# Kernel tuning notes

Hardware: AMD Instinct MI355X
Metric: run time of the kernel (lower is better)

Reference implementation:

```python
import jax, jax.numpy as jnp
import numpy as np

B, N, P, C, H = 8, 512, 16, 512, 8
HD = C // H  # 64


def setup_inputs() -> dict:
    key = jax.random.key(0)
    k1, k2, k3, k4, k5 = jax.random.split(key, 5)
    x = jax.random.normal(k1, (B, N, P, C), dtype=jnp.float32)
    # binary observation mask; force slot 0 valid so masked mean never divides by 0
    mask = (jax.random.uniform(k2, (B, N, P)) > 0.3).astype(jnp.float32)
    mask = mask.at[:, :, 0].set(1.0)
    lens = jax.random.randint(k3, (B,), 1, N)
    lens_mask = jnp.ones((B, N), dtype=jnp.float32)
    # parameters (torch Linear stored as [in, out] here; qkv_bias=False, proj has bias)
    Wqkv = jax.random.normal(k4, (C, 3 * C), dtype=jnp.float32) * (1.0 / np.sqrt(C))
    Wproj = jax.random.normal(k5, (C, C), dtype=jnp.float32) * (1.0 / np.sqrt(C))
    bproj = jnp.zeros((C,), dtype=jnp.float32)
    return {"x": x, "mask": mask, "lens": lens, "lens_mask": lens_mask,
            "Wqkv": Wqkv, "Wproj": Wproj, "bproj": bproj}


def reference(x, mask, lens, lens_mask, Wqkv, Wproj, bproj):
    # lens / lens_mask are unused by the original forward
    b, n, p, c = x.shape
    h, hd = H, c // H
    qkv = jnp.einsum('bnpc,cd->bnpd', x, Wqkv).reshape(b, n, p, 3, h, hd)
    # q: take P-slot 0                       -> [B,H,N,hd]
    q = qkv[:, :, 0, 0].transpose(0, 2, 1, 3)
    # k: masked mean over P                  -> [B,H,N,hd]
    m = mask[..., None, None]                      # [B,N,P,1,1]
    k = (jnp.where(m > 0, qkv[:, :, :, 1], 0.0).sum(axis=2) / m.sum(axis=2))
    k = k.transpose(0, 2, 1, 3)
    # v: pack P into channel dim             -> [B,H,N,hd*P]
    v = qkv[:, :, :, 2].transpose(0, 3, 1, 4, 2).reshape(b, h, n, hd * p)
    # SDPA over N (scale by 1/sqrt(head_dim of q))
    scale = 1.0 / np.sqrt(hd)
    attn = jax.nn.softmax(jnp.einsum('bhnd,bhmd->bhnm', q, k) * scale, axis=-1)
    out = jnp.einsum('bhnm,bhme->bhne', attn, v)            # [B,H,N,hd*P]
    # unpack P back out                       -> [B,N,P,C]
    out = out.reshape(b, h, n, hd, p).transpose(0, 2, 4, 1, 3).reshape(b, n, p, c)
    return out @ Wproj + bproj
```

## Files before the change

kernel.cpp:

```cpp
#include <hip/hip_runtime.h>

typedef _Float16 f16;
typedef __attribute__((ext_vector_type(8))) _Float16 half8;
typedef __attribute__((ext_vector_type(2))) _Float16 half2v;
typedef __attribute__((ext_vector_type(4))) float float4v;

#define MODE_QK 0
#define MODE_V 1
#define MODE_PV 2
#define MODE_PROJ 3


__device__ __forceinline__ void gload16(const f16* g, f16* l) {
    __builtin_amdgcn_global_load_lds(
        (const __attribute__((address_space(1))) void*)g,
        (__attribute__((address_space(3))) void*)l, 16, 0, 0);
}

__global__ __launch_bounds__(256) void wt_kernel(const float* __restrict__ Wqkv,
    const float* __restrict__ Wproj, f16* __restrict__ WT, f16* __restrict__ WpT)
{
    int idx = blockIdx.x * 256 + threadIdx.x;
    if (idx < 1536 * 512) {
        int d = idx >> 9, c = idx & 511;
        WT[idx] = (f16)Wqkv[c * 1536 + d];
    } else {
        int i2 = idx - 1536 * 512;
        int d = i2 >> 9, c = i2 & 511;
        WpT[i2] = (f16)Wproj[c * 512 + d];
    }
}

__global__ __launch_bounds__(256) void xprep_kernel(const float* __restrict__ x,
    const float* __restrict__ mask, f16* __restrict__ xf, f16* __restrict__ xmean)
{
    int bn = blockIdx.x;
    int t = threadIdx.x;
    const float* xrow = x + (size_t)bn * 16 * 512;
    const float* mrow = mask + (size_t)bn * 16;
    float msum = 0.f;
    #pragma unroll
    for (int p = 0; p < 16; p++) msum += mrow[p];
    int c = t * 2;
    float a0 = 0.f, a1 = 0.f;
    #pragma unroll
    for (int p = 0; p < 16; p++) {
        float2 v = *(const float2*)(xrow + p * 512 + c);
        float m = mrow[p];
        a0 += m * v.x; a1 += m * v.y;
        half2v h; h[0] = (f16)v.x; h[1] = (f16)v.y;
        *(half2v*)(xf + (size_t)bn * 16 * 512 + p * 512 + c) = h;
    }
    float inv = 1.f / msum;
    half2v hm; hm[0] = (f16)(a0 * inv); hm[1] = (f16)(a1 * inv);
    *(half2v*)(xmean + (size_t)bn * 512 + c) = hm;
}

template<int MODE>
__global__ __launch_bounds__(256) void gemm128(
    const f16* __restrict__ pA, const f16* __restrict__ pA2,
    const f16* __restrict__ pB,
    f16* __restrict__ outa, f16* __restrict__ outb,
    float* __restrict__ outf, const float* __restrict__ bias)
{
    __shared__ f16 As[128 * 32];
    __shared__ f16 Bs[128 * 32];
    const int t = threadIdx.x;
    const int lane = t & 63;
    const int w = t >> 6;
    const int wm = w & 1, wn = w >> 1;
    const int quad = lane >> 4, l15 = lane & 15;

    const int n0 = blockIdx.x * 128;
    const int m0 = blockIdx.y * 128;
    int vb = 0, vp = 0, z = 0;

    const f16* Abase; size_t sA;
    const f16* Bbase; size_t sB;
    if constexpr (MODE == MODE_QK) {
        if (n0 < 512) { Abase = pA;  sA = 8192; }
        else          { Abase = pA2; sA = 512;  }
        Bbase = pB; sB = 512;
    } else if constexpr (MODE == MODE_V) {
        z = blockIdx.z; vb = z >> 4; vp = z & 15;
        Abase = pA; sA = 512;
        Bbase = pB + ((size_t)vb * 512 * 16 + vp) * 512; sB = 8192;
    } else if constexpr (MODE == MODE_PV) {
        z = blockIdx.z;
        Abase = pA + (size_t)z * 512 * 512; sA = 512;
        Bbase = pB + (size_t)z * 1024 * 512; sB = 512;
    } else {
        Abase = pA; sA = 512;
        Bbase = pB; sB = 512;
    }

    const int rlo = (lane >> 2), kof = (lane & 3) * 8;
    const f16* ga0 = Abase + (size_t)(m0 + w * 16 + rlo) * sA + kof;
    const f16* ga1 = Abase + (size_t)(m0 + (w + 4) * 16 + rlo) * sA + kof;
    const f16* gb0 = Bbase + (size_t)(n0 + w * 16 + rlo) * sB + kof;
    const f16* gb1 = Bbase + (size_t)(n0 + (w + 4) * 16 + rlo) * sB + kof;
    f16* lA0 = As + w * 512;
    f16* lA1 = As + (w + 4) * 512;
    f16* lB0 = Bs + w * 512;
    f16* lB1 = Bs + (w + 4) * 512;

    float4v acc[4][4];
    #pragma unroll
    for (int i = 0; i < 4; i++)
        #pragma unroll
        for (int j = 0; j < 4; j++)
            acc[i][j] = (float4v){0.f, 0.f, 0.f, 0.f};

    for (int kt = 0; kt < 16; kt++) {
        __syncthreads();
        gload16(ga0, lA0); gload16(ga1, lA1);
        gload16(gb0, lB0); gload16(gb1, lB1);
        ga0 += 32; ga1 += 32; gb0 += 32; gb1 += 32;
        __syncthreads();
        half8 af[4], bf[4];
        #pragma unroll
        for (int mi = 0; mi < 4; mi++)
            af[mi] = *(const half8*)&As[(wm * 64 + mi * 16 + l15) * 32 + quad * 8];
        #pragma unroll
        for (int ni = 0; ni < 4; ni++)
            bf[ni] = *(const half8*)&Bs[(wn * 64 + ni * 16 + l15) * 32 + quad * 8];
        #pragma unroll
        for (int mi = 0; mi < 4; mi++)
            #pragma unroll
            for (int ni = 0; ni < 4; ni++)
                acc[mi][ni] = __builtin_amdgcn_mfma_f32_16x16x32_f16(
                    af[mi], bf[ni], acc[mi][ni], 0, 0, 0);
    }

    #pragma unroll
    for (int mi = 0; mi < 4; mi++) {
        #pragma unroll
        for (int ni = 0; ni < 4; ni++) {
            #pragma unroll
            for (int i = 0; i < 4; i++) {
                int lrow = wm * 64 + mi * 16 + quad * 4 + i;
                int lcol = wn * 64 + ni * 16 + l15;
                float val = acc[mi][ni][i];
                if constexpr (MODE == MODE_QK) {
                    int gm = m0 + lrow, gj = n0 + lcol;
                    int b = gm >> 9, n = gm & 511;
                    if (gj < 512)
                        outa[(((size_t)(b * 8 + (gj >> 6))) * 512 + n) * 64 + (gj & 63)] = (f16)val;
                    else {
                        int jj = gj - 512;
                        outb[(((size_t)(b * 8 + (jj >> 6))) * 512 + n) * 64 + (jj & 63)] = (f16)val;
                    }
                } else if constexpr (MODE == MODE_V) {
                    int gi = m0 + lrow, gn = n0 + lcol;
                    int h = gi >> 6, dd = gi & 63;
                    outa[(((size_t)(vb * 8 + h)) * 1024 + vp * 64 + dd) * 512 + gn] = (f16)val;
                } else if constexpr (MODE == MODE_PV) {
                    int n = m0 + lrow, e = n0 + lcol;
                    int p = e >> 6, dd = e & 63;
                    int b = z >> 3, h = z & 7;
                    outa[((size_t)(b * 512 + n) * 16 + p) * 512 + h * 64 + dd] = (f16)val;
                } else {
                    outf[(size_t)(m0 + lrow) * 512 + (n0 + lcol)] = val + bias[n0 + lcol];
                }
            }
        }
    }
}

__global__ __launch_bounds__(256) void qk_softmax_kernel(
    const f16* __restrict__ q, const f16* __restrict__ k, f16* __restrict__ Pout)
{
    __shared__ f16 qs[64 * 72];
    __shared__ f16 ks[512 * 72];
    const int t = threadIdx.x;
    const int bh = blockIdx.y;
    const int n0 = blockIdx.x * 64;
    #pragma unroll
    for (int i = 0; i < 2; i++) {
        int cid = i * 256 + t;
        int row = cid >> 3, off = (cid & 7) * 8;
        *(half8*)&qs[row * 72 + off] =
            *(const half8*)&q[((size_t)bh * 512 + n0 + row) * 64 + off];
    }
    #pragma unroll
    for (int i = 0; i < 16; i++) {
        int cid = i * 256 + t;
        int row = cid >> 3, off = (cid & 7) * 8;
        *(half8*)&ks[row * 72 + off] =
            *(const half8*)&k[((size_t)bh * 512 + row) * 64 + off];
    }
    __syncthreads();
    const int lane = t & 63, w = t >> 6;
    const int quad = lane >> 4, l15 = lane & 15;
    const int qrow = w * 16 + l15;
    half8 a0 = *(const half8*)&qs[qrow * 72 + quad * 8];
    half8 a1 = *(const half8*)&qs[qrow * 72 + 32 + quad * 8];
    float4v acc[32];
    #pragma unroll
    for (int f = 0; f < 32; f++) {
        int krow = f * 16 + l15;
        half8 b0 = *(const half8*)&ks[krow * 72 + quad * 8];
        half8 b1 = *(const half8*)&ks[krow * 72 + 32 + quad * 8];
        float4v c = {0.f, 0.f, 0.f, 0.f};
        c = __builtin_amdgcn_mfma_f32_16x16x32_f16(a0, b0, c, 0, 0, 0);
        c = __builtin_amdgcn_mfma_f32_16x16x32_f16(a1, b1, c, 0, 0, 0);
        acc[f] = c;
    }
    float mx0 = -3e38f, mx1 = -3e38f, mx2 = -3e38f, mx3 = -3e38f;
    #pragma unroll
    for (int f = 0; f < 32; f++) {
        mx0 = fmaxf(mx0, acc[f][0]); mx1 = fmaxf(mx1, acc[f][1]);
        mx2 = fmaxf(mx2, acc[f][2]); mx3 = fmaxf(mx3, acc[f][3]);
    }
    #pragma unroll
    for (int off = 1; off < 16; off <<= 1) {
        mx0 = fmaxf(mx0, __shfl_xor(mx0, off));
        mx1 = fmaxf(mx1, __shfl_xor(mx1, off));
        mx2 = fmaxf(mx2, __shfl_xor(mx2, off));
        mx3 = fmaxf(mx3, __shfl_xor(mx3, off));
    }
    float s0 = 0.f, s1 = 0.f, s2 = 0.f, s3 = 0.f;
    #pragma unroll
    for (int f = 0; f < 32; f++) {
        float e0 = __expf(0.125f * (acc[f][0] - mx0));
        float e1 = __expf(0.125f * (acc[f][1] - mx1));
        float e2 = __expf(0.125f * (acc[f][2] - mx2));
        float e3 = __expf(0.125f * (acc[f][3] - mx3));
        acc[f][0] = e0; acc[f][1] = e1; acc[f][2] = e2; acc[f][3] = e3;
        s0 += e0; s1 += e1; s2 += e2; s3 += e3;
    }
    #pragma unroll
    for (int off = 1; off < 16; off <<= 1) {
        s0 += __shfl_xor(s0, off);
        s1 += __shfl_xor(s1, off);
        s2 += __shfl_xor(s2, off);
        s3 += __shfl_xor(s3, off);
    }
    float r0 = 1.f / s0, r1 = 1.f / s1, r2 = 1.f / s2, r3 = 1.f / s3;
    size_t base = ((size_t)bh * 512 + n0 + w * 16) * 512;
    #pragma unroll
    for (int f = 0; f < 32; f++) {
        int col = f * 16 + l15;
        Pout[base + (size_t)(quad * 4 + 0) * 512 + col] = (f16)(acc[f][0] * r0);
        Pout[base + (size_t)(quad * 4 + 1) * 512 + col] = (f16)(acc[f][1] * r1);
        Pout[base + (size_t)(quad * 4 + 2) * 512 + col] = (f16)(acc[f][2] * r2);
        Pout[base + (size_t)(quad * 4 + 3) * 512 + col] = (f16)(acc[f][3] * r3);
    }
}

extern "C" void kernel_launch(void* const* d_in, const int* in_sizes, int n_in,
                              void* d_out, int out_size, void* d_ws, size_t ws_size,
                              hipStream_t stream)
{
    (void)in_sizes; (void)n_in; (void)out_size; (void)ws_size;
    const float* x     = (const float*)d_in[0];
    const float* mask  = (const float*)d_in[1];
    const float* Wqkv  = (const float*)d_in[4];
    const float* Wproj = (const float*)d_in[5];
    const float* bproj = (const float*)d_in[6];
    float* out = (float*)d_out;
    char* ws = (char*)d_ws;

    f16* xf16  = (f16*)(ws + 0);
    f16* vT    = (f16*)(ws + 67108864);
    f16* xmean = (f16*)(ws + 134217728);
    f16* WT    = (f16*)(ws + 138412032);
    f16* WpT   = (f16*)(ws + 139984896);
    f16* qb    = (f16*)(ws + 140509184);
    f16* kb    = (f16*)(ws + 144703488);
    f16* Pm    = (f16*)(ws + 148897792);
    f16* ypre  = xf16;

    wt_kernel<<<dim3(4096), dim3(256), 0, stream>>>(Wqkv, Wproj, WT, WpT);
    xprep_kernel<<<dim3(4096), dim3(256), 0, stream>>>(x, mask, xf16, xmean);
    gemm128<MODE_QK><<<dim3(8, 32), dim3(256), 0, stream>>>(
        xf16, xmean, WT, qb, kb, nullptr, nullptr);
    gemm128<MODE_V><<<dim3(4, 4, 128), dim3(256), 0, stream>>>(
        WT + 1024 * 512, nullptr, xf16, vT, nullptr, nullptr, nullptr);
    qk_softmax_kernel<<<dim3(8, 64), dim3(256), 0, stream>>>(qb, kb, Pm);
    gemm128<MODE_PV><<<dim3(8, 4, 64), dim3(256), 0, stream>>>(
        Pm, nullptr, vT, ypre, nullptr, nullptr, nullptr);
    gemm128<MODE_PROJ><<<dim3(4, 512), dim3(256), 0, stream>>>(
        ypre, nullptr, WpT, nullptr, nullptr, out, bproj);
}
```

Measured before the change: 442.7 us.

## Stage GEMM and softmax epilogues through LDS for vectorized stores; merge prep kernels

The GEMM epilogue now writes accumulators into shared memory and stores 16-byte vectors to global memory in place of scattered 2-byte stores. The projection output is written as float4 with the bias added. The QK-softmax kernel streams K in chunks through a swizzled LDS buffer using global_load_lds, and writes P through LDS staging so the stores are coalesced. The two preprocessing kernels are merged into one launch. In exchange the epilogues gain extra syncthreads and LDS round trips.

```diff
diff --git a/kernel.cpp b/kernel.cpp
--- a/kernel.cpp
+++ b/kernel.cpp
@@ -17,23 +17,24 @@
         (__attribute__((address_space(3))) void*)l, 16, 0, 0);
 }
 
-__global__ __launch_bounds__(256) void wt_kernel(const float* __restrict__ Wqkv,
-    const float* __restrict__ Wproj, f16* __restrict__ WT, f16* __restrict__ WpT)
+__global__ __launch_bounds__(256) void prep_kernel(
+    const float* __restrict__ x, const float* __restrict__ mask,
+    const float* __restrict__ Wqkv, const float* __restrict__ Wproj,
+    f16* __restrict__ xf, f16* __restrict__ xmean,
+    f16* __restrict__ WT, f16* __restrict__ WpT)
 {
-    int idx = blockIdx.x * 256 + threadIdx.x;
-    if (idx < 1536 * 512) {
-        int d = idx >> 9, c = idx & 511;
-        WT[idx] = (f16)Wqkv[c * 1536 + d];
-    } else {
-        int i2 = idx - 1536 * 512;
-        int d = i2 >> 9, c = i2 & 511;
-        WpT[i2] = (f16)Wproj[c * 512 + d];
-    }
-}
-
-__global__ __launch_bounds__(256) void xprep_kernel(const float* __restrict__ x,
-    const float* __restrict__ mask, f16* __restrict__ xf, f16* __restrict__ xmean)
-{
+    if (blockIdx.x >= 4096) {
+        int idx = (blockIdx.x - 4096) * 256 + threadIdx.x;
+        if (idx < 1536 * 512) {
+            int d = idx >> 9, c = idx & 511;
+            WT[idx] = (f16)Wqkv[c * 1536 + d];
+        } else {
+            int i2 = idx - 1536 * 512;
+            int d = i2 >> 9, c = i2 & 511;
+            WpT[i2] = (f16)Wproj[c * 512 + d];
+        }
+        return;
+    }
     int bn = blockIdx.x;
     int t = threadIdx.x;
     const float* xrow = x + (size_t)bn * 16 * 512;
@@ -63,8 +64,9 @@
     f16* __restrict__ outa, f16* __restrict__ outb,
     float* __restrict__ outf, const float* __restrict__ bias)
 {
-    __shared__ f16 As[128 * 32];
-    __shared__ f16 Bs[128 * 32];
+    __shared__ __align__(16) f16 sm[8192];
+    f16* As = sm;
+    f16* Bs = sm + 4096;
     const int t = threadIdx.x;
     const int lane = t & 63;
     const int w = t >> 6;
@@ -132,37 +134,73 @@
                     af[mi], bf[ni], acc[mi][ni], 0, 0, 0);
     }
 
-    #pragma unroll
-    for (int mi = 0; mi < 4; mi++) {
-        #pragma unroll
-        for (int ni = 0; ni < 4; ni++) {
+    __syncthreads();
+
+    if constexpr (MODE == MODE_PROJ) {
+        float* pf = (float*)sm;
+        const int rp = t >> 4, cp = (t & 15) * 8;
+        float4v bb0 = *(const float4v*)&bias[n0 + cp];
+        float4v bb1 = *(const float4v*)&bias[n0 + cp + 4];
+        #pragma unroll
+        for (int ci = 0; ci < 8; ci++) {
+            if (wm == (ci >> 2)) {
+                int mi = ci & 3;
+                #pragma unroll
+                for (int ni = 0; ni < 4; ni++)
+                    #pragma unroll
+                    for (int i = 0; i < 4; i++)
+                        pf[(quad * 4 + i) * 132 + wn * 64 + ni * 16 + l15] =
+                            acc[mi][ni][i];
+            }
+            __syncthreads();
+            float4v v0 = *(const float4v*)&pf[rp * 132 + cp];
+            float4v v1 = *(const float4v*)&pf[rp * 132 + cp + 4];
+            size_t gb = (size_t)(m0 + ci * 16 + rp) * 512 + n0 + cp;
+            *(float4v*)&outf[gb] = v0 + bb0;
+            *(float4v*)&outf[gb + 4] = v1 + bb1;
+            __syncthreads();
+        }
+    } else {
+        f16* ph = sm;
+        const int rp = t >> 3, cp = (t & 7) * 16;
+        #pragma unroll
+        for (int ci = 0; ci < 4; ci++) {
+            if (wm == (ci >> 1)) {
+                #pragma unroll
+                for (int mh = 0; mh < 2; mh++) {
+                    int mi = (ci & 1) * 2 + mh;
+                    #pragma unroll
+                    for (int ni = 0; ni < 4; ni++)
+                        #pragma unroll
+                        for (int i = 0; i < 4; i++)
+                            ph[(mh * 16 + quad * 4 + i) * 136 + wn * 64 + ni * 16 + l15] =
+                                (f16)acc[mi][ni][i];
+                }
+            }
+            __syncthreads();
+            int gr = m0 + ci * 32 + rp;
             #pragma unroll
-            for (int i = 0; i < 4; i++) {
-                int lrow = wm * 64 + mi * 16 + quad * 4 + i;
-                int lcol = wn * 64 + ni * 16 + l15;
-                float val = acc[mi][ni][i];
+            for (int s = 0; s < 2; s++) {
+                half8 v = *(const half8*)&ph[rp * 136 + cp + s * 8];
+                int gc = n0 + cp + s * 8;
                 if constexpr (MODE == MODE_QK) {
-                    int gm = m0 + lrow, gj = n0 + lcol;
-                    int b = gm >> 9, n = gm & 511;
-                    if (gj < 512)
-                        outa[(((size_t)(b * 8 + (gj >> 6))) * 512 + n) * 64 + (gj & 63)] = (f16)val;
+                    int b = gr >> 9, n = gr & 511;
+                    if (gc < 512)
+                        *(half8*)&outa[(((size_t)(b * 8 + (gc >> 6))) * 512 + n) * 64 + (gc & 63)] = v;
                     else {
-                        int jj = gj - 512;
-                        outb[(((size_t)(b * 8 + (jj >> 6))) * 512 + n) * 64 + (jj & 63)] = (f16)val;
+                        int jj = gc - 512;
+                        *(half8*)&outb[(((size_t)(b * 8 + (jj >> 6))) * 512 + n) * 64 + (jj & 63)] = v;
                     }
                 } else if constexpr (MODE == MODE_V) {
-                    int gi = m0 + lrow, gn = n0 + lcol;
-                    int h = gi >> 6, dd = gi & 63;
-                    outa[(((size_t)(vb * 8 + h)) * 1024 + vp * 64 + dd) * 512 + gn] = (f16)val;
-                } else if constexpr (MODE == MODE_PV) {
-                    int n = m0 + lrow, e = n0 + lcol;
-                    int p = e >> 6, dd = e & 63;
+                    int h = gr >> 6, dd = gr & 63;
+                    *(half8*)&outa[(((size_t)(vb * 8 + h)) * 1024 + vp * 64 + dd) * 512 + gc] = v;
+                } else {
+                    int p = gc >> 6, dd = gc & 63;
                     int b = z >> 3, h = z & 7;
-                    outa[((size_t)(b * 512 + n) * 16 + p) * 512 + h * 64 + dd] = (f16)val;
-                } else {
-                    outf[(size_t)(m0 + lrow) * 512 + (n0 + lcol)] = val + bias[n0 + lcol];
+                    *(half8*)&outa[((size_t)(b * 512 + gr) * 16 + p) * 512 + h * 64 + dd] = v;
                 }
             }
+            __syncthreads();
         }
     }
 }
@@ -170,42 +208,47 @@
 __global__ __launch_bounds__(256) void qk_softmax_kernel(
     const f16* __restrict__ q, const f16* __restrict__ k, f16* __restrict__ Pout)
 {
-    __shared__ f16 qs[64 * 72];
-    __shared__ f16 ks[512 * 72];
+    __shared__ __align__(16) f16 sm[16896];
     const int t = threadIdx.x;
+    const int lane = t & 63, w = t >> 6;
+    const int quad = lane >> 4, l15 = lane & 15;
     const int bh = blockIdx.y;
     const int n0 = blockIdx.x * 64;
-    #pragma unroll
-    for (int i = 0; i < 2; i++) {
-        int cid = i * 256 + t;
-        int row = cid >> 3, off = (cid & 7) * 8;
-        *(half8*)&qs[row * 72 + off] =
-            *(const half8*)&q[((size_t)bh * 512 + n0 + row) * 64 + off];
-    }
-    #pragma unroll
-    for (int i = 0; i < 16; i++) {
-        int cid = i * 256 + t;
-        int row = cid >> 3, off = (cid & 7) * 8;
-        *(half8*)&ks[row * 72 + off] =
-            *(const half8*)&k[((size_t)bh * 512 + row) * 64 + off];
-    }
-    __syncthreads();
-    const int lane = t & 63, w = t >> 6;
-    const int quad = lane >> 4, l15 = lane & 15;
-    const int qrow = w * 16 + l15;
-    half8 a0 = *(const half8*)&qs[qrow * 72 + quad * 8];
-    half8 a1 = *(const half8*)&qs[qrow * 72 + 32 + quad * 8];
+
+    const f16* kbase = k + (size_t)bh * 512 * 64;
+    const f16* qp = q + ((size_t)bh * 512 + n0 + w * 16 + l15) * 64 + quad * 8;
+    half8 a0 = *(const half8*)qp;
+    half8 a1 = *(const half8*)(qp + 32);
+
     float4v acc[32];
     #pragma unroll
-    for (int f = 0; f < 32; f++) {
-        int krow = f * 16 + l15;
-        half8 b0 = *(const half8*)&ks[krow * 72 + quad * 8];
-        half8 b1 = *(const half8*)&ks[krow * 72 + 32 + quad * 8];
-        float4v c = {0.f, 0.f, 0.f, 0.f};
-        c = __builtin_amdgcn_mfma_f32_16x16x32_f16(a0, b0, c, 0, 0, 0);
-        c = __builtin_amdgcn_mfma_f32_16x16x32_f16(a1, b1, c, 0, 0, 0);
-        acc[f] = c;
-    }
+    for (int f = 0; f < 32; f++) acc[f] = (float4v){0.f, 0.f, 0.f, 0.f};
+
+    const int srow = lane >> 3, scol = lane & 7;
+    #pragma unroll
+    for (int c = 0; c < 4; c++) {
+        __syncthreads();
+        #pragma unroll
+        for (int i = 0; i < 4; i++) {
+            int ci2 = w * 4 + i;
+            int row = ci2 * 8 + srow;
+            gload16(kbase + c * 8192 + row * 64 + ((scol ^ (row & 7)) << 3),
+                    sm + ci2 * 512 + lane * 8);
+        }
+        __syncthreads();
+        #pragma unroll
+        for (int fl = 0; fl < 8; fl++) {
+            int row16 = fl * 16 + l15;
+            int sw = row16 & 7;
+            half8 b0 = *(const half8*)&sm[row16 * 64 + ((quad ^ sw) << 3)];
+            half8 b1 = *(const half8*)&sm[row16 * 64 + (((quad + 4) ^ sw) << 3)];
+            acc[c * 8 + fl] = __builtin_amdgcn_mfma_f32_16x16x32_f16(
+                a0, b0, acc[c * 8 + fl], 0, 0, 0);
+            acc[c * 8 + fl] = __builtin_amdgcn_mfma_f32_16x16x32_f16(
+                a1, b1, acc[c * 8 + fl], 0, 0, 0);
+        }
+    }
+
     float mx0 = -3e38f, mx1 = -3e38f, mx2 = -3e38f, mx3 = -3e38f;
     #pragma unroll
     for (int f = 0; f < 32; f++) {
@@ -237,14 +280,26 @@
         s3 += __shfl_xor(s3, off);
     }
     float r0 = 1.f / s0, r1 = 1.f / s1, r2 = 1.f / s2, r3 = 1.f / s3;
-    size_t base = ((size_t)bh * 512 + n0 + w * 16) * 512;
-    #pragma unroll
-    for (int f = 0; f < 32; f++) {
-        int col = f * 16 + l15;
-        Pout[base + (size_t)(quad * 4 + 0) * 512 + col] = (f16)(acc[f][0] * r0);
-        Pout[base + (size_t)(quad * 4 + 1) * 512 + col] = (f16)(acc[f][1] * r1);
-        Pout[base + (size_t)(quad * 4 + 2) * 512 + col] = (f16)(acc[f][2] * r2);
-        Pout[base + (size_t)(quad * 4 + 3) * 512 + col] = (f16)(acc[f][3] * r3);
+
+    __syncthreads();
+    f16* pb = sm + w * 4224;
+    const int rr = lane >> 2, cb = (lane & 3) * 64;
+    #pragma unroll
+    for (int cc = 0; cc < 2; cc++) {
+        #pragma unroll
+        for (int ff = 0; ff < 16; ff++) {
+            int f = cc * 16 + ff;
+            pb[(quad * 4 + 0) * 264 + ff * 16 + l15] = (f16)(acc[f][0] * r0);
+            pb[(quad * 4 + 1) * 264 + ff * 16 + l15] = (f16)(acc[f][1] * r1);
+            pb[(quad * 4 + 2) * 264 + ff * 16 + l15] = (f16)(acc[f][2] * r2);
+            pb[(quad * 4 + 3) * 264 + ff * 16 + l15] = (f16)(acc[f][3] * r3);
+        }
+        size_t gb = ((size_t)bh * 512 + n0 + w * 16 + rr) * 512 + cc * 256 + cb;
+        #pragma unroll
+        for (int s = 0; s < 8; s++) {
+            half8 v = *(const half8*)&pb[rr * 264 + cb + s * 8];
+            *(half8*)&Pout[gb + s * 8] = v;
+        }
     }
 }
 
@@ -271,8 +326,8 @@
     f16* Pm    = (f16*)(ws + 148897792);
     f16* ypre  = xf16;
 
-    wt_kernel<<<dim3(4096), dim3(256), 0, stream>>>(Wqkv, Wproj, WT, WpT);
-    xprep_kernel<<<dim3(4096), dim3(256), 0, stream>>>(x, mask, xf16, xmean);
+    prep_kernel<<<dim3(8192), dim3(256), 0, stream>>>(
+        x, mask, Wqkv, Wproj, xf16, xmean, WT, WpT);
     gemm128<MODE_QK><<<dim3(8, 32), dim3(256), 0, stream>>>(
         xf16, xmean, WT, qb, kb, nullptr, nullptr);
     gemm128<MODE_V><<<dim3(4, 4, 128), dim3(256), 0, stream>>>(
```

Measured after the change: 467.4 us. 1.06x slower.
